# Kernel tuning notes

Hardware: AMD Instinct MI355X
Metric: run time of the kernel (lower is better)

## Reference

```python
import jax, jax.numpy as jnp
import numpy as np

B, T, C = 4, 2048, 1024
N_HEADS = 16
HEAD_DIM = C // N_HEADS

def setup_inputs() -> dict:
    key = jax.random.key(0)
    k1, k2, k3 = jax.random.split(key, 3)
    x = jax.random.normal(k1, (B, T, C), dtype=jnp.float32)
    w_attn = jax.random.normal(k2, (C, 3 * C), dtype=jnp.float32) * (1.0 / np.sqrt(C))
    b_attn = jnp.zeros((3 * C,), dtype=jnp.float32)
    w_proj = jax.random.normal(k3, (C, C), dtype=jnp.float32) * (1.0 / np.sqrt(C))
    b_proj = jnp.zeros((C,), dtype=jnp.float32)
    return {"x": x, "w_attn": w_attn, "b_attn": b_attn, "w_proj": w_proj, "b_proj": b_proj}

def reference(x, w_attn, b_attn, w_proj, b_proj):
    Bx, Tx, Cx = x.shape
    qkv = x @ w_attn + b_attn                      # [B,T,3C]
    q, k, v = jnp.split(qkv, 3, axis=-1)
    def heads(t):
        return t.reshape(Bx, Tx, N_HEADS, HEAD_DIM).transpose(0, 2, 1, 3)  # [B,H,T,D]
    q, k, v = heads(q), heads(k), heads(v)
    scale = 1.0 / np.sqrt(HEAD_DIM)
    attn = jnp.einsum('bhqd,bhkd->bhqk', q, k) * scale  # [B,H,T,T]
    causal = jnp.tril(jnp.ones((Tx, Tx), dtype=bool))
    attn = jnp.where(causal[None, None, :, :], attn, -jnp.inf)
    attn = jax.nn.softmax(attn, axis=-1)
    out = jnp.einsum('bhqk,bhkd->bhqd', attn, v)        # [B,H,T,D]
    out = out.transpose(0, 2, 1, 3).reshape(Bx, Tx, Cx)
    return out @ w_proj + b_proj
```

## Files before the change

### kernel.cpp

```cpp
#include <hip/hip_runtime.h>
#include <hip/hip_bf16.h>

#define BATCH 4
#define SEQ   2048
#define CH    1024
#define NH    16
#define HD    64
#define BT    8192

typedef __attribute__((ext_vector_type(8))) short bf16x8;
typedef __attribute__((ext_vector_type(4))) float f32x4;
typedef __attribute__((ext_vector_type(16))) float f32x16;

__device__ __forceinline__ unsigned short f2b(float f) {
  __hip_bfloat16 h = __float2bfloat16(f);
  return *reinterpret_cast<unsigned short*>(&h);
}

__device__ __forceinline__ unsigned cvt_pk(float lo, float hi_) {
  unsigned r;
  asm("v_cvt_pk_bf16_f32 %0, %1, %2" : "=v"(r) : "v"(lo), "v"(hi_));
  return r;
}
__device__ __forceinline__ void plane_swap(unsigned &a, unsigned &b) {
  asm("v_permlane32_swap_b32 %0, %1" : "+v"(a), "+v"(b));
}


__global__ void conv_x_bf16(const float* __restrict__ in, unsigned short* __restrict__ out, int n4) {
  int i = blockIdx.x * blockDim.x + threadIdx.x;
  if (i >= n4) return;
  float4 v = reinterpret_cast<const float4*>(in)[i];
  ushort4 o;
  o.x = f2b(v.x); o.y = f2b(v.y); o.z = f2b(v.z); o.w = f2b(v.w);
  reinterpret_cast<ushort4*>(out)[i] = o;
}

__global__ void transpose_w_bf16(const float* __restrict__ in, unsigned short* __restrict__ out,
                                 int R, int Cc) {
  __shared__ float tile[32][33];
  int c0 = blockIdx.x * 32, r0 = blockIdx.y * 32;
  int tx = threadIdx.x, ty = threadIdx.y;
  #pragma unroll
  for (int i = 0; i < 32; i += 8)
    tile[ty + i][tx] = in[(size_t)(r0 + ty + i) * Cc + c0 + tx];
  __syncthreads();
  #pragma unroll
  for (int i = 0; i < 32; i += 8)
    out[(size_t)(c0 + ty + i) * R + r0 + tx] = f2b(tile[tx][ty + i]);
}


#define QSCALE 0.18033688011112042f

#define GSTAGE(BUF, K0)                                                                        \
  {                                                                                            \
    _Pragma("unroll")                                                                          \
    for (int c = 0; c < 2; ++c) {                                                              \
      int idx = c * 256 + tid;                                                                 \
      const unsigned short* sA = A + (size_t)(m0 + (idx >> 2)) * 1024 + (K0) + (idx & 3) * 8;  \
      __builtin_amdgcn_global_load_lds((const __attribute__((address_space(1))) void*)sA,      \
          (__attribute__((address_space(3))) void*)&sb[(BUF) * 4096 + (c * 256 + (tid & ~63)) * 8], 16, 0, 0); \
      const unsigned short* sB = Bt + (size_t)(n0 + (idx >> 2)) * 1024 + (K0) + (idx & 3) * 8; \
      __builtin_amdgcn_global_load_lds((const __attribute__((address_space(1))) void*)sB,      \
          (__attribute__((address_space(3))) void*)&sb[12288 + (BUF) * 4096 + (c * 256 + (tid & ~63)) * 8], 16, 0, 0); \
    }                                                                                          \
  }

__global__ __launch_bounds__(256) void gemm_qkv(
    const unsigned short* __restrict__ A,
    const unsigned short* __restrict__ Bt,
    const float* __restrict__ bias,
    unsigned short* __restrict__ Qb,
    unsigned short* __restrict__ Kb,
    unsigned short* __restrict__ Vt) {
  __shared__ __align__(16) unsigned short sb[24576];
  int tid = threadIdx.x;
  int lane = tid & 63, wav = tid >> 6;
  int wr = wav >> 1, wc = wav & 1;
  int lr = lane & 15, lh = lane >> 4;
  int m0 = blockIdx.x * 128, n0 = blockIdx.y * 128;

  f32x4 acc[4][4];
  #pragma unroll
  for (int i = 0; i < 4; ++i)
    #pragma unroll
    for (int j = 0; j < 4; ++j)
      acc[i][j] = f32x4{0.f, 0.f, 0.f, 0.f};

  GSTAGE(0, 0)
  GSTAGE(1, 32)
  asm volatile("s_waitcnt vmcnt(4)" ::: "memory");
  __builtin_amdgcn_s_barrier();

  int cur = 0;
  for (int k0 = 0; k0 < 1024; k0 += 32) {
    bool issued = (k0 + 64 < 1024);
    int nb = cur + 2; if (nb >= 3) nb -= 3;
    if (issued) GSTAGE(nb, k0 + 64)
    bf16x8 a[4], b[4];
    #pragma unroll
    for (int i = 0; i < 4; ++i)
      a[i] = *reinterpret_cast<const bf16x8*>(&sb[cur * 4096 + (wr * 64 + i * 16 + lr) * 32 + lh * 8]);
    #pragma unroll
    for (int j = 0; j < 4; ++j)
      b[j] = *reinterpret_cast<const bf16x8*>(&sb[12288 + cur * 4096 + (wc * 64 + j * 16 + lr) * 32 + lh * 8]);
    #pragma unroll
    for (int i = 0; i < 4; ++i)
      #pragma unroll
      for (int j = 0; j < 4; ++j)
        acc[i][j] = __builtin_amdgcn_mfma_f32_16x16x32_bf16(a[i], b[j], acc[i][j], 0, 0, 0);
    if (issued) { asm volatile("s_waitcnt vmcnt(4)" ::: "memory"); }
    else        { asm volatile("s_waitcnt vmcnt(0)" ::: "memory"); }
    __builtin_amdgcn_s_barrier();
    cur = (cur + 1 == 3) ? 0 : cur + 1;
  }

  int which = n0 >> 10;
  int h2 = (n0 >> 6) & 15;
  int bb = m0 >> 11, t0 = m0 & 2047;

  if (which < 2) {
    unsigned short* dst = which ? Kb : Qb;
    float sc = which ? 1.0f : QSCALE;
    size_t headbase = (size_t)(bb * 16 + h2 + wc) * SEQ;
    #pragma unroll
    for (int j = 0; j < 4; ++j) {
      int d = j * 16 + lr;
      float bv = bias[n0 + wc * 64 + d];
      #pragma unroll
      for (int i = 0; i < 4; ++i) {
        #pragma unroll
        for (int r = 0; r < 4; ++r) {
          int t = t0 + wr * 64 + i * 16 + lh * 4 + r;
          dst[(headbase + t) * HD + d] = f2b((acc[i][j][r] + bv) * sc);
        }
      }
    }
  } else {
    unsigned short* tile = sb;
    #pragma unroll
    for (int half = 0; half < 2; ++half) {
      if (wc == half) {
        #pragma unroll
        for (int j = 0; j < 4; ++j) {
          int nrow = j * 16 + lr;
          float bv = bias[n0 + half * 64 + nrow];
          int sw = nrow & 7;
          #pragma unroll
          for (int i = 0; i < 4; ++i) {
            int cm = wr * 16 + i * 4 + lh;
            unsigned lo = cvt_pk(acc[i][j][0] + bv, acc[i][j][1] + bv);
            unsigned hi_ = cvt_pk(acc[i][j][2] + bv, acc[i][j][3] + bv);
            unsigned long long val = (unsigned long long)lo | ((unsigned long long)hi_ << 32);
            *reinterpret_cast<unsigned long long*>(&tile[nrow * 128 + (cm ^ sw) * 4]) = val;
          }
        }
      }
      __syncthreads();
      size_t vbase = (size_t)((bb * 16 + h2 + half) * 64);
      #pragma unroll
      for (int it = 0; it < 4; ++it) {
        int pid = it * 256 + tid;
        int nrow = pid >> 4, p = pid & 15;
        int sw = nrow & 7;
        union { unsigned long long u[2]; bf16x8 v; } u;
        u.u[0] = *reinterpret_cast<const unsigned long long*>(&tile[nrow * 128 + ((2 * p) ^ sw) * 4]);
        u.u[1] = *reinterpret_cast<const unsigned long long*>(&tile[nrow * 128 + (((2 * p) ^ sw) ^ 1) * 4]);
        *reinterpret_cast<bf16x8*>(&Vt[(vbase + nrow) * SEQ + t0 + p * 8]) = u.v;
      }
      __syncthreads();
    }
  }
}


__global__ __launch_bounds__(512, 2) void attn_fwd(
    const unsigned short* __restrict__ Qb,
    const unsigned short* __restrict__ Kb,
    const unsigned short* __restrict__ Vt,
    unsigned short* __restrict__ AO) {
  __shared__ __align__(16) unsigned short sbuf[32768];

  int tid = threadIdx.x;
  int lane = tid & 63, w = tid >> 6;
  int ql = lane & 31, hi = lane >> 5;
  int bid = blockIdx.x;
  int head = bid & 63;
  int qs = 7 - (bid >> 6);
  int q0 = qs * 256;
  int NT = 2 * (qs + 1);
  int b = head >> 4, h = head & 15;

  const unsigned short* Qh = Qb + (size_t)head * SEQ * HD;
  const unsigned short* Kh = Kb + (size_t)head * SEQ * HD;
  const unsigned short* Vh = Vt + (size_t)head * HD * SEQ;

#define STAGE128(BUF, KV0)                                                                     \
  {                                                                                            \
    _Pragma("unroll")                                                                          \
    for (int c = 0; c < 2; ++c) {                                                              \
      int idx = c * 512 + tid;                                                                 \
      int krow = idx >> 3;                                                                     \
      int kcg = (idx & 7) ^ (krow & 7);                                                        \
      const unsigned short* srcK_ = Kh + (size_t)((KV0) + krow) * HD + kcg * 8;                \
      __builtin_amdgcn_global_load_lds((const __attribute__((address_space(1))) void*)srcK_,   \
          (__attribute__((address_space(3))) void*)&sbuf[(BUF) * 8192 + (c * 512 + (tid & ~63)) * 8], 16, 0, 0); \
      int vrow = idx >> 4;                                                                     \
      int vcg = (idx & 15) ^ (vrow & 15);                                                      \
      const unsigned short* srcV_ = Vh + (size_t)vrow * SEQ + (KV0) + vcg * 8;                 \
      __builtin_amdgcn_global_load_lds((const __attribute__((address_space(1))) void*)srcV_,   \
          (__attribute__((address_space(3))) void*)&sbuf[16384 + (BUF) * 8192 + (c * 512 + (tid & ~63)) * 8], 16, 0, 0); \
    }                                                                                          \
  }

  int qg = q0 + w * 32 + ql;
  bf16x8 qf[4];
  #pragma unroll
  for (int dblk = 0; dblk < 4; ++dblk)
    qf[dblk] = *reinterpret_cast<const bf16x8*>(&Qh[(size_t)qg * HD + dblk * 16 + hi * 8]);

  f32x16 o0 = (f32x16)0.0f, o1 = (f32x16)0.0f;
  float mrun = -1e30f, lrun = 0.f;

  STAGE128(0, 0)
  asm volatile("s_waitcnt vmcnt(0)" ::: "memory");
  __builtin_amdgcn_s_barrier();

  int cur = 0;
  int wq_hi = q0 + w * 32 + 31;
  for (int t = 0; t < NT; ++t) {
    int tkv0 = t * 128;
    if (t + 1 < NT) STAGE128(cur ^ 1, tkv0 + 128)

    #pragma unroll
    for (int sub = 0; sub < 2; ++sub) {
      int kv0 = tkv0 + sub * 64;
      if (kv0 <= wq_hi) {
        f32x16 s0 = (f32x16)0.0f, s1 = (f32x16)0.0f;
        int rk0 = sub * 64 + ql, rk1 = sub * 64 + 32 + ql;
        __builtin_amdgcn_s_setprio(1);
        #pragma unroll
        for (int dblk = 0; dblk < 4; ++dblk) {
          bf16x8 kf0 = *reinterpret_cast<const bf16x8*>(
              &sbuf[cur * 8192 + rk0 * 64 + (((dblk * 2 + hi) ^ (rk0 & 7)) << 3)]);
          s0 = __builtin_amdgcn_mfma_f32_32x32x16_bf16(kf0, qf[dblk], s0, 0, 0, 0);
          bf16x8 kf1 = *reinterpret_cast<const bf16x8*>(
              &sbuf[cur * 8192 + rk1 * 64 + (((dblk * 2 + hi) ^ (rk1 & 7)) << 3)]);
          s1 = __builtin_amdgcn_mfma_f32_32x32x16_bf16(kf1, qf[dblk], s1, 0, 0, 0);
        }
        __builtin_amdgcn_s_setprio(0);

        float p[32];
        bool needMask = (kv0 + 63 > q0 + 32 * w);
        #pragma unroll
        for (int r = 0; r < 16; ++r) {
          int cr = (r & 3) + 8 * (r >> 2);
          float v0 = s0[r], v1 = s1[r];
          if (needMask) {
            int kv_ = kv0 + 4 * hi + cr;
            v0 = (kv_ > qg) ? -1e30f : v0;
            v1 = (kv_ + 32 > qg) ? -1e30f : v1;
          }
          p[r] = v0; p[16 + r] = v1;
        }

        float m16[16], m8[8], m4[4], m2[2];
        #pragma unroll
        for (int i = 0; i < 16; ++i) m16[i] = fmaxf(p[i], p[i + 16]);
        #pragma unroll
        for (int i = 0; i < 8; ++i) m8[i] = fmaxf(m16[i], m16[i + 8]);
        #pragma unroll
        for (int i = 0; i < 4; ++i) m4[i] = fmaxf(m8[i], m8[i + 4]);
        m2[0] = fmaxf(m4[0], m4[2]); m2[1] = fmaxf(m4[1], m4[3]);
        float mt = fmaxf(m2[0], m2[1]);
        mt = fmaxf(mt, __shfl_xor(mt, 32));
        float mnew = fmaxf(mrun, mt);
        float alpha = __builtin_amdgcn_exp2f(mrun - mnew);
        mrun = mnew;

        #pragma unroll
        for (int i = 0; i < 32; ++i) p[i] = __builtin_amdgcn_exp2f(p[i] - mnew);
        float a16[16], a8[8], a4[4];
        #pragma unroll
        for (int i = 0; i < 16; ++i) a16[i] = p[i] + p[i + 16];
        #pragma unroll
        for (int i = 0; i < 8; ++i) a8[i] = a16[i] + a16[i + 8];
        #pragma unroll
        for (int i = 0; i < 4; ++i) a4[i] = a8[i] + a8[i + 4];
        float rs = (a4[0] + a4[1]) + (a4[2] + a4[3]);
        rs += __shfl_xor(rs, 32);
        lrun = lrun * alpha + rs;

        #pragma unroll
        for (int i = 0; i < 16; ++i) { o0[i] *= alpha; o1[i] *= alpha; }

        union FU { unsigned u[4]; bf16x8 v; };
        FU fr[4];
        #pragma unroll
        for (int blk = 0; blk < 2; ++blk) {
          unsigned X = cvt_pk(p[blk * 16 + 0], p[blk * 16 + 1]);
          unsigned Z = cvt_pk(p[blk * 16 + 4], p[blk * 16 + 5]);
          plane_swap(X, Z);
          unsigned Y = cvt_pk(p[blk * 16 + 2], p[blk * 16 + 3]);
          unsigned W = cvt_pk(p[blk * 16 + 6], p[blk * 16 + 7]);
          plane_swap(Y, W);
          fr[blk * 2].u[0] = X; fr[blk * 2].u[1] = Y; fr[blk * 2].u[2] = Z; fr[blk * 2].u[3] = W;
          unsigned X2 = cvt_pk(p[blk * 16 + 8], p[blk * 16 + 9]);
          unsigned Z2 = cvt_pk(p[blk * 16 + 12], p[blk * 16 + 13]);
          plane_swap(X2, Z2);
          unsigned Y2 = cvt_pk(p[blk * 16 + 10], p[blk * 16 + 11]);
          unsigned W2 = cvt_pk(p[blk * 16 + 14], p[blk * 16 + 15]);
          plane_swap(Y2, W2);
          fr[blk * 2 + 1].u[0] = X2; fr[blk * 2 + 1].u[1] = Y2;
          fr[blk * 2 + 1].u[2] = Z2; fr[blk * 2 + 1].u[3] = W2;
        }

        __builtin_amdgcn_s_setprio(1);
        #pragma unroll
        for (int kc = 0; kc < 4; ++kc) {
          int rd0 = ql, rd1 = 32 + ql;
          int gch = sub * 8 + (kc << 1) + hi;
          bf16x8 vf0 = *reinterpret_cast<const bf16x8*>(
              &sbuf[16384 + cur * 8192 + rd0 * 128 + ((gch ^ (rd0 & 15)) << 3)]);
          o0 = __builtin_amdgcn_mfma_f32_32x32x16_bf16(vf0, fr[kc].v, o0, 0, 0, 0);
          bf16x8 vf1 = *reinterpret_cast<const bf16x8*>(
              &sbuf[16384 + cur * 8192 + rd1 * 128 + ((gch ^ (rd1 & 15)) << 3)]);
          o1 = __builtin_amdgcn_mfma_f32_32x32x16_bf16(vf1, fr[kc].v, o1, 0, 0, 0);
        }
        __builtin_amdgcn_s_setprio(0);
      }
    }

    asm volatile("s_waitcnt vmcnt(0)" ::: "memory");
    __builtin_amdgcn_s_barrier();
    cur ^= 1;
  }

  float inv = 1.0f / lrun;
  int qloc = w * 32 + ql;
  #pragma unroll
  for (int dblk = 0; dblk < 2; ++dblk) {
    #pragma unroll
    for (int m = 0; m < 4; ++m) {
      float v0, v1, v2, v3;
      if (dblk == 0) {
        v0 = o0[m * 4 + 0] * inv; v1 = o0[m * 4 + 1] * inv;
        v2 = o0[m * 4 + 2] * inv; v3 = o0[m * 4 + 3] * inv;
      } else {
        v0 = o1[m * 4 + 0] * inv; v1 = o1[m * 4 + 1] * inv;
        v2 = o1[m * 4 + 2] * inv; v3 = o1[m * 4 + 3] * inv;
      }
      unsigned u0 = (unsigned)f2b(v0) | ((unsigned)f2b(v1) << 16);
      unsigned u1 = (unsigned)f2b(v2) | ((unsigned)f2b(v3) << 16);
      int slot = (dblk * 4 + m) ^ (qloc & 7);
      unsigned long long val = (unsigned long long)u0 | ((unsigned long long)u1 << 32);
      *reinterpret_cast<unsigned long long*>(&sbuf[qloc * 64 + slot * 8 + hi * 4]) = val;
    }
  }
  __syncthreads();

  #pragma unroll
  for (int it = 0; it < 4; ++it) {
    int qr = it * 64 + (tid >> 3);
    int lc = tid & 7;
    int slot = lc ^ (qr & 7);
    bf16x8 v = *reinterpret_cast<const bf16x8*>(&sbuf[qr * 64 + slot * 8]);
    *reinterpret_cast<bf16x8*>(
        &AO[(size_t)(b * SEQ + q0 + qr) * CH + h * 64 + lc * 8]) = v;
  }
}


__global__ __launch_bounds__(256) void gemm_proj(
    const unsigned short* __restrict__ A,
    const unsigned short* __restrict__ Bt,
    const float* __restrict__ bias,
    float* __restrict__ out) {
  __shared__ __align__(16) unsigned short sb[24576];
  int tid = threadIdx.x;
  int lane = tid & 63, wav = tid >> 6;
  int wr = wav >> 1, wc = wav & 1;
  int lr = lane & 15, lh = lane >> 4;
  int m0 = blockIdx.x * 128, n0 = blockIdx.y * 128;

  f32x4 acc[4][4];
  #pragma unroll
  for (int i = 0; i < 4; ++i)
    #pragma unroll
    for (int j = 0; j < 4; ++j)
      acc[i][j] = f32x4{0.f, 0.f, 0.f, 0.f};

  GSTAGE(0, 0)
  GSTAGE(1, 32)
  asm volatile("s_waitcnt vmcnt(4)" ::: "memory");
  __builtin_amdgcn_s_barrier();

  int cur = 0;
  for (int k0 = 0; k0 < 1024; k0 += 32) {
    bool issued = (k0 + 64 < 1024);
    int nb = cur + 2; if (nb >= 3) nb -= 3;
    if (issued) GSTAGE(nb, k0 + 64)
    bf16x8 a[4], b[4];
    #pragma unroll
    for (int i = 0; i < 4; ++i)
      a[i] = *reinterpret_cast<const bf16x8*>(&sb[cur * 4096 + (wr * 64 + i * 16 + lr) * 32 + lh * 8]);
    #pragma unroll
    for (int j = 0; j < 4; ++j)
      b[j] = *reinterpret_cast<const bf16x8*>(&sb[12288 + cur * 4096 + (wc * 64 + j * 16 + lr) * 32 + lh * 8]);
    #pragma unroll
    for (int i = 0; i < 4; ++i)
      #pragma unroll
      for (int j = 0; j < 4; ++j)
        acc[i][j] = __builtin_amdgcn_mfma_f32_16x16x32_bf16(a[i], b[j], acc[i][j], 0, 0, 0);
    if (issued) { asm volatile("s_waitcnt vmcnt(4)" ::: "memory"); }
    else        { asm volatile("s_waitcnt vmcnt(0)" ::: "memory"); }
    __builtin_amdgcn_s_barrier();
    cur = (cur + 1 == 3) ? 0 : cur + 1;
  }

  #pragma unroll
  for (int i = 0; i < 4; ++i) {
    #pragma unroll
    for (int j = 0; j < 4; ++j) {
      int n = n0 + wc * 64 + j * 16 + lr;
      float bv = bias[n];
      #pragma unroll
      for (int r = 0; r < 4; ++r) {
        int m = m0 + wr * 64 + i * 16 + lh * 4 + r;
        out[(size_t)m * 1024 + n] = acc[i][j][r] + bv;
      }
    }
  }
}


extern "C" void kernel_launch(void* const* d_in, const int* in_sizes, int n_in,
                              void* d_out, int out_size, void* d_ws, size_t ws_size,
                              hipStream_t stream) {
  const float* x      = (const float*)d_in[0];
  const float* w_attn = (const float*)d_in[1];
  const float* b_attn = (const float*)d_in[2];
  const float* w_proj = (const float*)d_in[3];
  const float* b_proj = (const float*)d_in[4];
  float* out = (float*)d_out;

  char* ws = (char*)d_ws;
  unsigned short* xb  = (unsigned short*)(ws);
  unsigned short* wAT = (unsigned short*)(ws + 16777216);
  unsigned short* wPT = (unsigned short*)(ws + 23068672);
  unsigned short* Qb  = (unsigned short*)(ws + 25165824);
  unsigned short* Kb  = (unsigned short*)(ws + 41943040);
  unsigned short* Vt  = (unsigned short*)(ws + 58720256);
  unsigned short* AO  = (unsigned short*)(ws + 75497472);

  conv_x_bf16<<<(BT * CH / 4 + 255) / 256, 256, 0, stream>>>(x, xb, BT * CH / 4);
  transpose_w_bf16<<<dim3(3 * CH / 32, CH / 32), dim3(32, 8), 0, stream>>>(w_attn, wAT, CH, 3 * CH);
  transpose_w_bf16<<<dim3(CH / 32, CH / 32), dim3(32, 8), 0, stream>>>(w_proj, wPT, CH, CH);
  gemm_qkv<<<dim3(BT / 128, 3 * CH / 128), 256, 0, stream>>>(xb, wAT, b_attn, Qb, Kb, Vt);
  attn_fwd<<<512, 512, 0, stream>>>(Qb, Kb, Vt, AO);
  gemm_proj<<<dim3(BT / 128, CH / 128), 256, 0, stream>>>(AO, wPT, b_proj, out);
}
```

Measured before the change: 164.7 us.

## Use BK=64 double-buffered GEMM with XOR-swizzled LDS layout

```diff
diff --git a/kernel.cpp b/kernel.cpp
--- a/kernel.cpp
+++ b/kernel.cpp
@@ -53,18 +53,53 @@
 
 #define QSCALE 0.18033688011112042f
 
-#define GSTAGE(BUF, K0)                                                                        \
+#define GSTAGE64(BUF, K0)                                                                      \
   {                                                                                            \
     _Pragma("unroll")                                                                          \
-    for (int c = 0; c < 2; ++c) {                                                              \
+    for (int c = 0; c < 4; ++c) {                                                              \
       int idx = c * 256 + tid;                                                                 \
-      const unsigned short* sA = A + (size_t)(m0 + (idx >> 2)) * 1024 + (K0) + (idx & 3) * 8;  \
+      int row = idx >> 3;                                                                      \
+      int cg = (idx & 7) ^ (row & 7);                                                          \
+      const unsigned short* sA = A + (size_t)(m0 + row) * 1024 + (K0) + cg * 8;                \
       __builtin_amdgcn_global_load_lds((const __attribute__((address_space(1))) void*)sA,      \
-          (__attribute__((address_space(3))) void*)&sb[(BUF) * 4096 + (c * 256 + (tid & ~63)) * 8], 16, 0, 0); \
-      const unsigned short* sB = Bt + (size_t)(n0 + (idx >> 2)) * 1024 + (K0) + (idx & 3) * 8; \
+          (__attribute__((address_space(3))) void*)&sb[(BUF) * 8192 + (c * 256 + (tid & ~63)) * 8], 16, 0, 0); \
+      const unsigned short* sB = Bt + (size_t)(n0 + row) * 1024 + (K0) + cg * 8;               \
       __builtin_amdgcn_global_load_lds((const __attribute__((address_space(1))) void*)sB,      \
-          (__attribute__((address_space(3))) void*)&sb[12288 + (BUF) * 4096 + (c * 256 + (tid & ~63)) * 8], 16, 0, 0); \
+          (__attribute__((address_space(3))) void*)&sb[16384 + (BUF) * 8192 + (c * 256 + (tid & ~63)) * 8], 16, 0, 0); \
     }                                                                                          \
+  }
+
+#define GEMM_MAIN_LOOP                                                                         \
+  GSTAGE64(0, 0)                                                                               \
+  asm volatile("s_waitcnt vmcnt(0)" ::: "memory");                                             \
+  __builtin_amdgcn_s_barrier();                                                                \
+  int cur = 0;                                                                                 \
+  for (int k0 = 0; k0 < 1024; k0 += 64) {                                                      \
+    if (k0 + 64 < 1024) GSTAGE64(cur ^ 1, k0 + 64)                                             \
+    _Pragma("unroll")                                                                          \
+    for (int sub = 0; sub < 2; ++sub) {                                                        \
+      bf16x8 a[4], b[4];                                                                       \
+      _Pragma("unroll")                                                                        \
+      for (int i = 0; i < 4; ++i) {                                                            \
+        int row = wr * 64 + i * 16 + lr;                                                       \
+        a[i] = *reinterpret_cast<const bf16x8*>(                                               \
+            &sb[cur * 8192 + row * 64 + (((sub * 4 + lh) ^ (lr & 7)) << 3)]);                  \
+      }                                                                                        \
+      _Pragma("unroll")                                                                        \
+      for (int j = 0; j < 4; ++j) {                                                            \
+        int row = wc * 64 + j * 16 + lr;                                                       \
+        b[j] = *reinterpret_cast<const bf16x8*>(                                               \
+            &sb[16384 + cur * 8192 + row * 64 + (((sub * 4 + lh) ^ (lr & 7)) << 3)]);          \
+      }                                                                                        \
+      _Pragma("unroll")                                                                        \
+      for (int i = 0; i < 4; ++i)                                                              \
+        _Pragma("unroll")                                                                      \
+        for (int j = 0; j < 4; ++j)                                                            \
+          acc[i][j] = __builtin_amdgcn_mfma_f32_16x16x32_bf16(a[i], b[j], acc[i][j], 0, 0, 0); \
+    }                                                                                          \
+    asm volatile("s_waitcnt vmcnt(0)" ::: "memory");                                           \
+    __builtin_amdgcn_s_barrier();                                                              \
+    cur ^= 1;                                                                                  \
   }
 
 __global__ __launch_bounds__(256) void gemm_qkv(
@@ -74,7 +109,7 @@
     unsigned short* __restrict__ Qb,
     unsigned short* __restrict__ Kb,
     unsigned short* __restrict__ Vt) {
-  __shared__ __align__(16) unsigned short sb[24576];
+  __shared__ __align__(16) unsigned short sb[32768];
   int tid = threadIdx.x;
   int lane = tid & 63, wav = tid >> 6;
   int wr = wav >> 1, wc = wav & 1;
@@ -88,33 +123,7 @@
     for (int j = 0; j < 4; ++j)
       acc[i][j] = f32x4{0.f, 0.f, 0.f, 0.f};
 
-  GSTAGE(0, 0)
-  GSTAGE(1, 32)
-  asm volatile("s_waitcnt vmcnt(4)" ::: "memory");
-  __builtin_amdgcn_s_barrier();
-
-  int cur = 0;
-  for (int k0 = 0; k0 < 1024; k0 += 32) {
-    bool issued = (k0 + 64 < 1024);
-    int nb = cur + 2; if (nb >= 3) nb -= 3;
-    if (issued) GSTAGE(nb, k0 + 64)
-    bf16x8 a[4], b[4];
-    #pragma unroll
-    for (int i = 0; i < 4; ++i)
-      a[i] = *reinterpret_cast<const bf16x8*>(&sb[cur * 4096 + (wr * 64 + i * 16 + lr) * 32 + lh * 8]);
-    #pragma unroll
-    for (int j = 0; j < 4; ++j)
-      b[j] = *reinterpret_cast<const bf16x8*>(&sb[12288 + cur * 4096 + (wc * 64 + j * 16 + lr) * 32 + lh * 8]);
-    #pragma unroll
-    for (int i = 0; i < 4; ++i)
-      #pragma unroll
-      for (int j = 0; j < 4; ++j)
-        acc[i][j] = __builtin_amdgcn_mfma_f32_16x16x32_bf16(a[i], b[j], acc[i][j], 0, 0, 0);
-    if (issued) { asm volatile("s_waitcnt vmcnt(4)" ::: "memory"); }
-    else        { asm volatile("s_waitcnt vmcnt(0)" ::: "memory"); }
-    __builtin_amdgcn_s_barrier();
-    cur = (cur + 1 == 3) ? 0 : cur + 1;
-  }
+  GEMM_MAIN_LOOP
 
   int which = n0 >> 10;
   int h2 = (n0 >> 6) & 15;
@@ -140,36 +149,30 @@
   } else {
     unsigned short* tile = sb;
     #pragma unroll
-    for (int half = 0; half < 2; ++half) {
-      if (wc == half) {
-        #pragma unroll
-        for (int j = 0; j < 4; ++j) {
-          int nrow = j * 16 + lr;
-          float bv = bias[n0 + half * 64 + nrow];
-          int sw = nrow & 7;
-          #pragma unroll
-          for (int i = 0; i < 4; ++i) {
-            int cm = wr * 16 + i * 4 + lh;
-            unsigned lo = cvt_pk(acc[i][j][0] + bv, acc[i][j][1] + bv);
-            unsigned hi_ = cvt_pk(acc[i][j][2] + bv, acc[i][j][3] + bv);
-            unsigned long long val = (unsigned long long)lo | ((unsigned long long)hi_ << 32);
-            *reinterpret_cast<unsigned long long*>(&tile[nrow * 128 + (cm ^ sw) * 4]) = val;
-          }
-        }
+    for (int j = 0; j < 4; ++j) {
+      int d = wc * 64 + j * 16 + lr;
+      float bv = bias[n0 + d];
+      int sw = d & 7;
+      #pragma unroll
+      for (int i = 0; i < 4; ++i) {
+        int cm = wr * 16 + i * 4 + lh;
+        unsigned lo = cvt_pk(acc[i][j][0] + bv, acc[i][j][1] + bv);
+        unsigned hi_ = cvt_pk(acc[i][j][2] + bv, acc[i][j][3] + bv);
+        unsigned long long val = (unsigned long long)lo | ((unsigned long long)hi_ << 32);
+        *reinterpret_cast<unsigned long long*>(&tile[d * 128 + ((cm ^ sw) << 2)]) = val;
       }
-      __syncthreads();
-      size_t vbase = (size_t)((bb * 16 + h2 + half) * 64);
-      #pragma unroll
-      for (int it = 0; it < 4; ++it) {
-        int pid = it * 256 + tid;
-        int nrow = pid >> 4, p = pid & 15;
-        int sw = nrow & 7;
-        union { unsigned long long u[2]; bf16x8 v; } u;
-        u.u[0] = *reinterpret_cast<const unsigned long long*>(&tile[nrow * 128 + ((2 * p) ^ sw) * 4]);
-        u.u[1] = *reinterpret_cast<const unsigned long long*>(&tile[nrow * 128 + (((2 * p) ^ sw) ^ 1) * 4]);
-        *reinterpret_cast<bf16x8*>(&Vt[(vbase + nrow) * SEQ + t0 + p * 8]) = u.v;
-      }
-      __syncthreads();
+    }
+    __syncthreads();
+    #pragma unroll
+    for (int it = 0; it < 8; ++it) {
+      int pid = it * 256 + tid;
+      int drow = pid >> 4, p = pid & 15;
+      int sw = drow & 7;
+      union { unsigned long long u[2]; bf16x8 v; } u;
+      u.u[0] = *reinterpret_cast<const unsigned long long*>(&tile[drow * 128 + (((2 * p) ^ sw) << 2)]);
+      u.u[1] = *reinterpret_cast<const unsigned long long*>(&tile[drow * 128 + ((((2 * p) ^ sw) ^ 1) << 2)]);
+      *reinterpret_cast<bf16x8*>(
+          &Vt[((size_t)(bb * 16 + h2 + (drow >> 6)) * 64 + (drow & 63)) * SEQ + t0 + p * 8]) = u.v;
     }
   }
 }
@@ -377,7 +380,7 @@
     const unsigned short* __restrict__ Bt,
     const float* __restrict__ bias,
     float* __restrict__ out) {
-  __shared__ __align__(16) unsigned short sb[24576];
+  __shared__ __align__(16) unsigned short sb[32768];
   int tid = threadIdx.x;
   int lane = tid & 63, wav = tid >> 6;
   int wr = wav >> 1, wc = wav & 1;
@@ -391,33 +394,7 @@
     for (int j = 0; j < 4; ++j)
       acc[i][j] = f32x4{0.f, 0.f, 0.f, 0.f};
 
-  GSTAGE(0, 0)
-  GSTAGE(1, 32)
-  asm volatile("s_waitcnt vmcnt(4)" ::: "memory");
-  __builtin_amdgcn_s_barrier();
-
-  int cur = 0;
-  for (int k0 = 0; k0 < 1024; k0 += 32) {
-    bool issued = (k0 + 64 < 1024);
-    int nb = cur + 2; if (nb >= 3) nb -= 3;
-    if (issued) GSTAGE(nb, k0 + 64)
-    bf16x8 a[4], b[4];
-    #pragma unroll
-    for (int i = 0; i < 4; ++i)
-      a[i] = *reinterpret_cast<const bf16x8*>(&sb[cur * 4096 + (wr * 64 + i * 16 + lr) * 32 + lh * 8]);
-    #pragma unroll
-    for (int j = 0; j < 4; ++j)
-      b[j] = *reinterpret_cast<const bf16x8*>(&sb[12288 + cur * 4096 + (wc * 64 + j * 16 + lr) * 32 + lh * 8]);
-    #pragma unroll
-    for (int i = 0; i < 4; ++i)
-      #pragma unroll
-      for (int j = 0; j < 4; ++j)
-        acc[i][j] = __builtin_amdgcn_mfma_f32_16x16x32_bf16(a[i], b[j], acc[i][j], 0, 0, 0);
-    if (issued) { asm volatile("s_waitcnt vmcnt(4)" ::: "memory"); }
-    else        { asm volatile("s_waitcnt vmcnt(0)" ::: "memory"); }
-    __builtin_amdgcn_s_barrier();
-    cur = (cur + 1 == 3) ? 0 : cur + 1;
-  }
+  GEMM_MAIN_LOOP
 
   #pragma unroll
   for (int i = 0; i < 4; ++i) {
```

After: 155.9 us. 1.06x faster.
